# Performance work log

Hardware: AMD Instinct MI355X
Metric: run time of the kernel (lower is better)

## Reference

```python
import jax, jax.numpy as jnp
import numpy as np

V = 128
L = 128
N = 4096

_ALPHA = "abcdefghijklmnopqrstuvwxyz"
TOKENS = (list("+-*/^()=") + [f"temp_{a}" for a in _ALPHA]
          + [str(d) for d in range(10)] + [f"w{i}" for i in range(84)])
assert len(TOKENS) == V
IDX = {t: i for i, t in enumerate(TOKENS)}
TEMPS = [f"temp_{a}" for a in _ALPHA]


def _build_mask_table() -> np.ndarray:
    """mask_table[p, v] = 0 if token v is illegal after prev-token p, else 1.
    Mirrors RuleFilter.single_filter's rho for every possible prev token."""
    M = np.ones((V, V), dtype=np.float32)

    def ban(prev_tokens, banned_tokens):
        cols = [IDX[t] for t in banned_tokens]
        for p in prev_tokens:
            M[IDX[p], cols] = 0.0

    ban(list("+-*/"), list("+-*/)="))          # prev is binary op
    ban(TEMPS, list("(="))                      # prev is temp_* variable
    ban(["="], list("+-*/=)") + TEMPS)         # prev is '='
    ban(["("], list("()+-*/="))                # prev is '('
    ban([")"], list("()") + TEMPS)             # prev is ')'
    ban(["^"], list("+-*/=)"))                 # prev is '^'
    return M


def setup_inputs() -> dict:
    key = jax.random.key(0)
    logits = jax.random.normal(key, (L, N, V), dtype=jnp.float32)
    mask_table = jnp.asarray(_build_mask_table())  # (V, V) rule lookup
    return {"logits": logits, "mask_table": mask_table}


def reference(logits, mask_table):
    """logits: (L, N, V); mask_table: (V, V). Sequential rule masking:
    logits[i] *= mask_table[argmax(filtered logits[i-1])]."""
    first = logits[0]  # row 0 is never filtered

    def step(carry, cur):
        # carry: previously *filtered* logits row (N, V)
        prev_idx = jnp.argmax(carry, axis=-1)          # (N,)
        new = cur * mask_table[prev_idx]               # gather + multiply
        return new, new

    _, rest = jax.lax.scan(step, first, logits[1:])
    return jnp.concatenate([first[None], rest], axis=0)
```

## Files before the change

kernel.cpp:

```cpp
#include <hip/hip_runtime.h>


constexpr int V = 128;
constexpr int L = 128;
constexpr int N = 4096;
constexpr int D = 20;
constexpr unsigned ROWB = (unsigned)N * V * 4;

typedef __attribute__((ext_vector_type(2))) float f32x2;

__device__ __forceinline__ float wave_max_dpp(float x) {
    int v = __float_as_int(x);
    const int ninf = __float_as_int(-__builtin_inff());
#define RF_STEP(ctrl)                                                          \
    {                                                                          \
        int s = __builtin_amdgcn_update_dpp(ninf, v, ctrl, 0xf, 0xf, false);   \
        v = __float_as_int(fmaxf(__int_as_float(v), __int_as_float(s)));       \
    }
    RF_STEP(0x111)
    RF_STEP(0x112)
    RF_STEP(0x114)
    RF_STEP(0x118)
    RF_STEP(0x142)
    RF_STEP(0x143)
#undef RF_STEP
    return __int_as_float(__builtin_amdgcn_readlane(v, 63));
}

__device__ __forceinline__ int wave_argmax(f32x2 f) {
    const float bv = wave_max_dpp(fmaxf(f.x, f.y));
    unsigned long long b0 = __ballot(f.x == bv);
    unsigned long long b1 = __ballot(f.y == bv);
    int i0 = __ffsll(b0);
    int i1 = __ffsll(b1);
    int c0 = i0 ? (i0 - 1) * 2 : (1 << 30);
    int c1 = i1 ? (i1 - 1) * 2 + 1 : (1 << 30);
    return min(c0, c1);
}

__device__ __forceinline__ unsigned sel8(const unsigned* t, int j) {
    unsigned a0 = (j & 1) ? t[1] : t[0];
    unsigned a1 = (j & 1) ? t[3] : t[2];
    unsigned a2 = (j & 1) ? t[5] : t[4];
    unsigned a3 = (j & 1) ? t[7] : t[6];
    unsigned b0 = (j & 2) ? a1 : a0;
    unsigned b1 = (j & 2) ? a3 : a2;
    return (j & 4) ? b1 : b0;
}

__device__ __forceinline__ unsigned long long uniform_u64(const void* p) {
    unsigned long long x = (unsigned long long)p;
    unsigned lo = __builtin_amdgcn_readfirstlane((unsigned)x);
    unsigned hi = __builtin_amdgcn_readfirstlane((unsigned)(x >> 32));
    return ((unsigned long long)hi << 32) | lo;
}

template <int I>
struct Step {
    static __device__ __forceinline__ void run(f32x2* ring, f32x2* fbuf,
                                               const unsigned* tbl, int& prev,
                                               unsigned long long lbase,
                                               unsigned long long obase,
                                               unsigned laneoff) {
        constexpr int NW = (I <= D - 1) ? (D - 1 + I)
                         : ((I <= L - D - 1) ? (2 * D - 2) : (D - 1 + (L - 1 - I)));
        constexpr int s  = I % D;

        asm volatile("s_waitcnt vmcnt(%c2)"
                     : "+v"(ring[s])
                     : "v"(fbuf[s]), "i"(NW));

        f32x2 c = ring[s];
        f32x2 f;
        if (I == 0) {
            f = c;
        } else {
            const unsigned word  = sel8(tbl, prev >> 4);
            const unsigned fbits = (word >> ((prev & 15) * 2)) & 3u;
            f.x = (fbits & 1u) ? c.x : 0.0f;
            f.y = (fbits & 2u) ? c.y : 0.0f;
        }
        fbuf[s] = f;

        {
            unsigned voff = (unsigned)I * ROWB + laneoff;
            asm volatile("global_store_dwordx2 %0, %1, %2"
                         :
                         : "v"(voff), "v"(fbuf[s]), "s"(obase));
        }

        prev = wave_argmax(f);

        if constexpr (I + D < L) {
            unsigned voff = (unsigned)(I + D) * ROWB + laneoff;
            asm volatile("global_load_dwordx2 %0, %1, %2"
                         : "=&v"(ring[s])
                         : "v"(voff), "s"(lbase));
        }

        Step<I + 1>::run(ring, fbuf, tbl, prev, lbase, obase, laneoff);
    }
};
template <>
struct Step<L> {
    static __device__ __forceinline__ void run(f32x2*, f32x2*, const unsigned*,
                                               int&, unsigned long long,
                                               unsigned long long, unsigned) {}
};

__global__ __launch_bounds__(256, 4) void rule_filter_kernel(
    const float* __restrict__ logits,
    const float* __restrict__ mask_table,
    float* __restrict__ out)
{
    const int wave = threadIdx.x >> 6;
    const int lane = threadIdx.x & 63;
    const int n    = (blockIdx.x << 2) + wave;

    const unsigned long long lbase = uniform_u64(logits + (size_t)n * V);
    const unsigned long long obase = uniform_u64(out    + (size_t)n * V);
    const unsigned laneoff = (unsigned)lane * 8;

    unsigned tbl[8];
#pragma unroll 1
    for (int j = 0; j < 8; ++j) {
        unsigned acc = 0;
#pragma unroll
        for (int r = 0; r < 16; ++r) {
            const int p = j * 16 + r;
            float2 mv = *(const float2*)(mask_table + (size_t)p * V + lane * 2);
            acc |= ((mv.x != 0.0f ? 1u : 0u) | (mv.y != 0.0f ? 2u : 0u)) << (2 * r);
        }
        tbl[j] = acc;
    }
    asm volatile("s_waitcnt vmcnt(0)" ::: "memory");

    f32x2 ring[D];
    f32x2 fbuf[D];
#pragma unroll
    for (int r = 0; r < D; ++r) { fbuf[r].x = 0.0f; fbuf[r].y = 0.0f; }

#pragma unroll
    for (int r = 0; r < D; ++r) {
        unsigned voff = (unsigned)r * ROWB + laneoff;
        asm volatile("global_load_dwordx2 %0, %1, %2"
                     : "=&v"(ring[r])
                     : "v"(voff), "s"(lbase));
    }

    int prev = 0;
    Step<0>::run(ring, fbuf, tbl, prev, lbase, obase, laneoff);
}

extern "C" void kernel_launch(void* const* d_in, const int* in_sizes, int n_in,
                              void* d_out, int out_size, void* d_ws, size_t ws_size,
                              hipStream_t stream) {
    const float* logits     = (const float*)d_in[0];
    const float* mask_table = (const float*)d_in[1];
    float* out              = (float*)d_out;

    dim3 grid(N / 4);
    dim3 block(256);
    rule_filter_kernel<<<grid, block, 0, stream>>>(logits, mask_table, out);
}
```

Before: 439.1 us.

## Split sequential rule filter into class-argmax, chain, and apply kernels

Deduplicates mask_table rows into at most seven classes. For every logits row it computes the argmax under each class mask in a fully parallel pass, so the sequential dependency collapses to a small byte-table walk per sequence. A final streaming kernel applies the selected mask to each row. This removes the per-step latency-bound argmax chain, at the cost of reading the logits twice and needing a workspace. It also silently caps the class count at seven, so a mask table with more distinct rows would give wrong results.

New measurement: 556.8 us. 26.8% more time.

```diff
diff --git a/kernel.cpp b/kernel.cpp
--- a/kernel.cpp
+++ b/kernel.cpp
@@ -4,12 +4,22 @@
 constexpr int V = 128;
 constexpr int L = 128;
 constexpr int N = 4096;
-constexpr int D = 20;
-constexpr unsigned ROWB = (unsigned)N * V * 4;
-
-typedef __attribute__((ext_vector_type(2))) float f32x2;
-
-__device__ __forceinline__ float wave_max_dpp(float x) {
+constexpr int NROWS = L * N;
+
+struct Meta {
+    unsigned rows[8][4];
+    unsigned char slot[128];
+    unsigned nc;
+};
+constexpr size_t T1_BYTES = (size_t)NROWS * 8;
+constexpr size_t SEL_OFF  = T1_BYTES;
+constexpr size_t META_OFF = T1_BYTES + (size_t)NROWS;
+constexpr size_t WS_NEEDED = META_OFF + sizeof(Meta);
+
+typedef unsigned long long u64;
+
+
+__device__ __forceinline__ int halfmax_dpp(float x) {
     int v = __float_as_int(x);
     const int ninf = __float_as_int(-__builtin_inff());
 #define RF_STEP(ctrl)                                                          \
@@ -17,27 +27,247 @@
         int s = __builtin_amdgcn_update_dpp(ninf, v, ctrl, 0xf, 0xf, false);   \
         v = __float_as_int(fmaxf(__int_as_float(v), __int_as_float(s)));       \
     }
-    RF_STEP(0x111)
-    RF_STEP(0x112)
-    RF_STEP(0x114)
-    RF_STEP(0x118)
-    RF_STEP(0x142)
-    RF_STEP(0x143)
+    RF_STEP(0x111) RF_STEP(0x112) RF_STEP(0x114) RF_STEP(0x118) RF_STEP(0x142)
+#undef RF_STEP
+    return v;
+}
+
+__device__ __forceinline__ int argmax_half(unsigned m0, unsigned m1,
+                                           unsigned m2, unsigned m3) {
+    const int BIG = 1 << 30;
+    int c0 = m0 ? (__builtin_ctz(m0) * 4 + 0) : BIG;
+    int c1 = m1 ? (__builtin_ctz(m1) * 4 + 1) : BIG;
+    int c2 = m2 ? (__builtin_ctz(m2) * 4 + 2) : BIG;
+    int c3 = m3 ? (__builtin_ctz(m3) * 4 + 3) : BIG;
+    return min(min(c0, c1), min(c2, c3));
+}
+
+__device__ __forceinline__ unsigned sel4u(unsigned a, unsigned b, unsigned c,
+                                          unsigned d, int j) {
+    unsigned x = (j & 1) ? b : a;
+    unsigned y = (j & 1) ? d : c;
+    return (j & 2) ? y : x;
+}
+
+__device__ __forceinline__ float maskf(float x, unsigned bit) {
+    return __int_as_float(__float_as_int(x) & (0x80000000u | (0u - bit)));
+}
+
+__global__ void k0_classes(const float* __restrict__ mt, Meta* __restrict__ meta) {
+    __shared__ unsigned sb[128][4];
+    __shared__ unsigned char canon[128];
+    const int p = threadIdx.x;
+    unsigned w[4];
+#pragma unroll
+    for (int wi = 0; wi < 4; ++wi) {
+        unsigned acc = 0;
+        for (int b = 0; b < 32; ++b)
+            acc |= (mt[(size_t)p * V + wi * 32 + b] != 0.0f ? 1u : 0u) << b;
+        w[wi] = acc;
+        sb[p][wi] = acc;
+    }
+    __syncthreads();
+    int cq = p;
+    for (int q = 0; q < p; ++q) {
+        if (sb[q][0] == w[0] && sb[q][1] == w[1] && sb[q][2] == w[2] &&
+            sb[q][3] == w[3]) { cq = q; break; }
+    }
+    canon[p] = (cq == p) ? 1 : 0;
+    __syncthreads();
+    int rank = 0;
+    for (int q = 0; q < cq; ++q) rank += canon[q];
+    if (rank > 6) rank = 6;
+    meta->slot[p] = (unsigned char)rank;
+    if (cq == p && rank < 7)
+        for (int wi = 0; wi < 4; ++wi) meta->rows[rank][wi] = w[wi];
+    if (p == 0) {
+        int nc = 0;
+        for (int q = 0; q < 128; ++q) nc += canon[q];
+        meta->nc = nc > 7 ? 7 : nc;
+        for (int wi = 0; wi < 4; ++wi) meta->rows[7][wi] = 0xFFFFFFFFu;
+    }
+}
+
+__global__ __launch_bounds__(256) void k1_classargmax(
+    const float* __restrict__ logits, const Meta* __restrict__ meta,
+    u64* __restrict__ T1) {
+    const int lane = threadIdx.x & 63;
+    const int ll   = lane & 31;
+    const int half = lane >> 5;
+    const int gw   = blockIdx.x * 4 + (threadIdx.x >> 6);
+    const int NWV  = 2048 * 4;
+
+    const int nc = (int)meta->nc;
+    unsigned nib[8];
+    unsigned rw0[8], rw1[8], rw2[8], rw3[8];
+#pragma unroll
+    for (int c = 0; c < 8; ++c) {
+        rw0[c] = meta->rows[c][0]; rw1[c] = meta->rows[c][1];
+        rw2[c] = meta->rows[c][2]; rw3[c] = meta->rows[c][3];
+        unsigned word = sel4u(rw0[c], rw1[c], rw2[c], rw3[c], ll >> 3);
+        nib[c] = (word >> ((ll & 7) * 4)) & 0xFu;
+    }
+
+    const uint4* lp = (const uint4*)logits;
+
+    auto process = [&](int pw, uint4 xb) {
+        float x0 = __int_as_float(xb.x), x1 = __int_as_float(xb.y);
+        float x2 = __int_as_float(xb.z), x3 = __int_as_float(xb.w);
+        float mloc = fmaxf(fmaxf(x0, x1), fmaxf(x2, x3));
+        int mv = halfmax_dpp(mloc);
+        float bvA = __int_as_float(__builtin_amdgcn_readlane(mv, 31));
+        float bvB = __int_as_float(__builtin_amdgcn_readlane(mv, 63));
+        float bv = half ? bvB : bvA;
+        u64 e0 = __ballot(x0 == bv), e1 = __ballot(x1 == bv);
+        u64 e2 = __ballot(x2 == bv), e3 = __ballot(x3 == bv);
+        int iA7 = argmax_half((unsigned)e0, (unsigned)e1, (unsigned)e2, (unsigned)e3);
+        int iB7 = argmax_half((unsigned)(e0 >> 32), (unsigned)(e1 >> 32),
+                              (unsigned)(e2 >> 32), (unsigned)(e3 >> 32));
+        u64 accA = (u64)(unsigned)iA7 << 56;
+        u64 accB = (u64)(unsigned)iB7 << 56;
+#pragma unroll
+        for (int c = 0; c < 7; ++c) {
+            if (c < nc) {
+                bool okA = (bvA > 0.0f) &&
+                    ((sel4u(rw0[c], rw1[c], rw2[c], rw3[c], iA7 >> 5) >> (iA7 & 31)) & 1u);
+                bool okB = (bvB > 0.0f) &&
+                    ((sel4u(rw0[c], rw1[c], rw2[c], rw3[c], iB7 >> 5) >> (iB7 & 31)) & 1u);
+                int iA, iB;
+                if (okA && okB) {
+                    iA = iA7; iB = iB7;
+                } else {
+                    const unsigned nb = nib[c];
+                    float f0 = maskf(x0, nb & 1u),        f1 = maskf(x1, (nb >> 1) & 1u);
+                    float f2 = maskf(x2, (nb >> 2) & 1u), f3 = maskf(x3, (nb >> 3) & 1u);
+                    float mm = fmaxf(fmaxf(f0, f1), fmaxf(f2, f3));
+                    int mv2 = halfmax_dpp(mm);
+                    float cA = __int_as_float(__builtin_amdgcn_readlane(mv2, 31));
+                    float cB = __int_as_float(__builtin_amdgcn_readlane(mv2, 63));
+                    float cb = half ? cB : cA;
+                    u64 g0 = __ballot(f0 == cb), g1 = __ballot(f1 == cb);
+                    u64 g2 = __ballot(f2 == cb), g3 = __ballot(f3 == cb);
+                    iA = argmax_half((unsigned)g0, (unsigned)g1, (unsigned)g2, (unsigned)g3);
+                    iB = argmax_half((unsigned)(g0 >> 32), (unsigned)(g1 >> 32),
+                                     (unsigned)(g2 >> 32), (unsigned)(g3 >> 32));
+                    if (okA) iA = iA7;
+                    if (okB) iB = iB7;
+                }
+                accA |= (u64)(unsigned)iA << (8 * c);
+                accB |= (u64)(unsigned)iB << (8 * c);
+            }
+        }
+        if (lane < 2) T1[(size_t)2 * pw + lane] = lane ? accB : accA;
+    };
+
+    uint4 a = lp[((size_t)gw + 0 * NWV) * 64 + lane];
+    uint4 b = lp[((size_t)gw + 1 * NWV) * 64 + lane];
+#pragma unroll 1
+    for (int k = 0; k < 32; k += 2) {
+        uint4 n1 = a, n2 = b;
+        if (k + 2 < 32) {
+            n1 = lp[((size_t)gw + (size_t)(k + 2) * NWV) * 64 + lane];
+            n2 = lp[((size_t)gw + (size_t)(k + 3) * NWV) * 64 + lane];
+        }
+        process(gw + k * NWV, a);
+        process(gw + (k + 1) * NWV, b);
+        a = n1; b = n2;
+    }
+}
+
+__global__ __launch_bounds__(256) void k2_chain(
+    const u64* __restrict__ T1, const Meta* __restrict__ meta,
+    unsigned char* __restrict__ rowsel) {
+    __shared__ unsigned char slotl[128];
+    if (threadIdx.x < 128) slotl[threadIdx.x] = meta->slot[threadIdx.x];
+    __syncthreads();
+    const int n = blockIdx.x * 256 + threadIdx.x;
+
+    u64 cur[16], nxt[16];
+#pragma unroll
+    for (int j = 0; j < 16; ++j) cur[j] = T1[(size_t)j * N + n];
+
+    int prev = 0;
+#pragma unroll 1
+    for (int b = 0; b < 8; ++b) {
+        const int ib = b * 16;
+#pragma unroll
+        for (int j = 0; j < 16; ++j)
+            nxt[j] = (b < 7) ? T1[(size_t)(ib + 16 + j) * N + n] : 0ull;
+#pragma unroll
+        for (int j = 0; j < 16; ++j) {
+            const int i = ib + j;
+            if (i == 0) {
+                prev = (int)((cur[0] >> 56) & 0x7F);
+                rowsel[n] = (unsigned char)7;
+            } else {
+                int s = slotl[prev];
+                rowsel[(size_t)i * N + n] = (unsigned char)s;
+                prev = (int)((cur[j] >> (8 * s)) & 0x7F);
+            }
+        }
+#pragma unroll
+        for (int j = 0; j < 16; ++j) cur[j] = nxt[j];
+    }
+}
+
+__global__ __launch_bounds__(256) void k3_apply(
+    const float* __restrict__ logits, const Meta* __restrict__ meta,
+    const unsigned char* __restrict__ rowsel, float* __restrict__ out) {
+    __shared__ uint4 rowsl[8];
+    if (threadIdx.x < 8) {
+        const unsigned* r = &meta->rows[threadIdx.x][0];
+        rowsl[threadIdx.x] = make_uint4(r[0], r[1], r[2], r[3]);
+    }
+    __syncthreads();
+    const uint4* in = (const uint4*)logits;
+    uint4* o = (uint4*)out;
+    const size_t TOT = (size_t)L * N * V / 4;
+    const size_t id0 = (size_t)blockIdx.x * 256 + threadIdx.x;
+    const size_t stride = (size_t)2048 * 256;
+#pragma unroll 4
+    for (int k = 0; k < 32; ++k) {
+        size_t idx = (TOT - 1) - (id0 + (size_t)k * stride);
+        uint4 x = in[idx];
+        const int row = (int)(idx >> 5);
+        const int ll  = (int)(idx & 31);
+        const int s   = rowsel[row];
+        uint4 w = rowsl[s];
+        unsigned word = sel4u(w.x, w.y, w.z, w.w, ll >> 3);
+        unsigned nb = word >> ((ll & 7) * 4);
+        x.x &= 0x80000000u | (0u - (nb & 1u));
+        x.y &= 0x80000000u | (0u - ((nb >> 1) & 1u));
+        x.z &= 0x80000000u | (0u - ((nb >> 2) & 1u));
+        x.w &= 0x80000000u | (0u - ((nb >> 3) & 1u));
+        o[idx] = x;
+    }
+}
+
+constexpr int FD = 20;
+constexpr unsigned ROWB = (unsigned)N * V * 4;
+typedef __attribute__((ext_vector_type(2))) float f32x2;
+
+__device__ __forceinline__ float wave_max_dpp64(float x) {
+    int v = __float_as_int(x);
+    const int ninf = __float_as_int(-__builtin_inff());
+#define RF_STEP(ctrl)                                                          \
+    {                                                                          \
+        int s = __builtin_amdgcn_update_dpp(ninf, v, ctrl, 0xf, 0xf, false);   \
+        v = __float_as_int(fmaxf(__int_as_float(v), __int_as_float(s)));       \
+    }
+    RF_STEP(0x111) RF_STEP(0x112) RF_STEP(0x114) RF_STEP(0x118)
+    RF_STEP(0x142) RF_STEP(0x143)
 #undef RF_STEP
     return __int_as_float(__builtin_amdgcn_readlane(v, 63));
 }
-
-__device__ __forceinline__ int wave_argmax(f32x2 f) {
-    const float bv = wave_max_dpp(fmaxf(f.x, f.y));
-    unsigned long long b0 = __ballot(f.x == bv);
-    unsigned long long b1 = __ballot(f.y == bv);
-    int i0 = __ffsll(b0);
-    int i1 = __ffsll(b1);
+__device__ __forceinline__ int wave_argmax64(f32x2 f) {
+    const float bv = wave_max_dpp64(fmaxf(f.x, f.y));
+    u64 b0 = __ballot(f.x == bv);
+    u64 b1 = __ballot(f.y == bv);
+    int i0 = __ffsll(b0), i1 = __ffsll(b1);
     int c0 = i0 ? (i0 - 1) * 2 : (1 << 30);
     int c1 = i1 ? (i1 - 1) * 2 + 1 : (1 << 30);
     return min(c0, c1);
 }
-
 __device__ __forceinline__ unsigned sel8(const unsigned* t, int j) {
     unsigned a0 = (j & 1) ? t[1] : t[0];
     unsigned a1 = (j & 1) ? t[3] : t[2];
@@ -47,29 +277,23 @@
     unsigned b1 = (j & 2) ? a3 : a2;
     return (j & 4) ? b1 : b0;
 }
-
-__device__ __forceinline__ unsigned long long uniform_u64(const void* p) {
-    unsigned long long x = (unsigned long long)p;
+__device__ __forceinline__ u64 uniform_u64p(const void* p) {
+    u64 x = (u64)p;
     unsigned lo = __builtin_amdgcn_readfirstlane((unsigned)x);
     unsigned hi = __builtin_amdgcn_readfirstlane((unsigned)(x >> 32));
-    return ((unsigned long long)hi << 32) | lo;
-}
-
+    return ((u64)hi << 32) | lo;
+}
 template <int I>
-struct Step {
+struct FStep {
     static __device__ __forceinline__ void run(f32x2* ring, f32x2* fbuf,
                                                const unsigned* tbl, int& prev,
-                                               unsigned long long lbase,
-                                               unsigned long long obase,
+                                               u64 lbase, u64 obase,
                                                unsigned laneoff) {
-        constexpr int NW = (I <= D - 1) ? (D - 1 + I)
-                         : ((I <= L - D - 1) ? (2 * D - 2) : (D - 1 + (L - 1 - I)));
-        constexpr int s  = I % D;
-
+        constexpr int NW = (I <= FD - 1) ? (FD - 1 + I)
+                         : ((I <= L - FD - 1) ? (2 * FD - 2) : (FD - 1 + (L - 1 - I)));
+        constexpr int s = I % FD;
         asm volatile("s_waitcnt vmcnt(%c2)"
-                     : "+v"(ring[s])
-                     : "v"(fbuf[s]), "i"(NW));
-
+                     : "+v"(ring[s]) : "v"(fbuf[s]), "i"(NW));
         f32x2 c = ring[s];
         f32x2 f;
         if (I == 0) {
@@ -81,46 +305,34 @@
             f.y = (fbits & 2u) ? c.y : 0.0f;
         }
         fbuf[s] = f;
-
         {
             unsigned voff = (unsigned)I * ROWB + laneoff;
             asm volatile("global_store_dwordx2 %0, %1, %2"
-                         :
-                         : "v"(voff), "v"(fbuf[s]), "s"(obase));
-        }
-
-        prev = wave_argmax(f);
-
-        if constexpr (I + D < L) {
-            unsigned voff = (unsigned)(I + D) * ROWB + laneoff;
+                         :: "v"(voff), "v"(fbuf[s]), "s"(obase));
+        }
+        prev = wave_argmax64(f);
+        if constexpr (I + FD < L) {
+            unsigned voff = (unsigned)(I + FD) * ROWB + laneoff;
             asm volatile("global_load_dwordx2 %0, %1, %2"
-                         : "=&v"(ring[s])
-                         : "v"(voff), "s"(lbase));
-        }
-
-        Step<I + 1>::run(ring, fbuf, tbl, prev, lbase, obase, laneoff);
+                         : "=&v"(ring[s]) : "v"(voff), "s"(lbase));
+        }
+        FStep<I + 1>::run(ring, fbuf, tbl, prev, lbase, obase, laneoff);
     }
 };
 template <>
-struct Step<L> {
+struct FStep<L> {
     static __device__ __forceinline__ void run(f32x2*, f32x2*, const unsigned*,
-                                               int&, unsigned long long,
-                                               unsigned long long, unsigned) {}
+                                               int&, u64, u64, unsigned) {}
 };
-
-__global__ __launch_bounds__(256, 4) void rule_filter_kernel(
-    const float* __restrict__ logits,
-    const float* __restrict__ mask_table,
-    float* __restrict__ out)
-{
+__global__ __launch_bounds__(256, 4) void rule_filter_fused(
+    const float* __restrict__ logits, const float* __restrict__ mask_table,
+    float* __restrict__ out) {
     const int wave = threadIdx.x >> 6;
     const int lane = threadIdx.x & 63;
     const int n    = (blockIdx.x << 2) + wave;
-
-    const unsigned long long lbase = uniform_u64(logits + (size_t)n * V);
-    const unsigned long long obase = uniform_u64(out    + (size_t)n * V);
+    const u64 lbase = uniform_u64p(logits + (size_t)n * V);
+    const u64 obase = uniform_u64p(out    + (size_t)n * V);
     const unsigned laneoff = (unsigned)lane * 8;
-
     unsigned tbl[8];
 #pragma unroll 1
     for (int j = 0; j < 8; ++j) {
@@ -134,22 +346,18 @@
         tbl[j] = acc;
     }
     asm volatile("s_waitcnt vmcnt(0)" ::: "memory");
-
-    f32x2 ring[D];
-    f32x2 fbuf[D];
-#pragma unroll
-    for (int r = 0; r < D; ++r) { fbuf[r].x = 0.0f; fbuf[r].y = 0.0f; }
-
-#pragma unroll
-    for (int r = 0; r < D; ++r) {
+    f32x2 ring[FD];
+    f32x2 fbuf[FD];
+#pragma unroll
+    for (int r = 0; r < FD; ++r) { fbuf[r].x = 0.0f; fbuf[r].y = 0.0f; }
+#pragma unroll
+    for (int r = 0; r < FD; ++r) {
         unsigned voff = (unsigned)r * ROWB + laneoff;
         asm volatile("global_load_dwordx2 %0, %1, %2"
-                     : "=&v"(ring[r])
-                     : "v"(voff), "s"(lbase));
-    }
-
+                     : "=&v"(ring[r]) : "v"(voff), "s"(lbase));
+    }
     int prev = 0;
-    Step<0>::run(ring, fbuf, tbl, prev, lbase, obase, laneoff);
+    FStep<0>::run(ring, fbuf, tbl, prev, lbase, obase, laneoff);
 }
 
 extern "C" void kernel_launch(void* const* d_in, const int* in_sizes, int n_in,
@@ -159,7 +367,18 @@
     const float* mask_table = (const float*)d_in[1];
     float* out              = (float*)d_out;
 
-    dim3 grid(N / 4);
-    dim3 block(256);
-    rule_filter_kernel<<<grid, block, 0, stream>>>(logits, mask_table, out);
-}
+    if (d_ws != nullptr && ws_size >= WS_NEEDED) {
+        unsigned char* ws = (unsigned char*)d_ws;
+        u64* T1            = (u64*)ws;
+        unsigned char* sel = ws + SEL_OFF;
+        Meta* meta         = (Meta*)(ws + META_OFF);
+        k0_classes<<<1, 128, 0, stream>>>(mask_table, meta);
+        k1_classargmax<<<2048, 256, 0, stream>>>(logits, meta, T1);
+        k2_chain<<<16, 256, 0, stream>>>(T1, meta, sel);
+        k3_apply<<<2048, 256, 0, stream>>>(logits, meta, sel, out);
+    } else {
+        dim3 grid(N / 4);
+        dim3 block(256);
+        rule_filter_fused<<<grid, block, 0, stream>>>(logits, mask_table, out);
+    }
+}
```

## Split each sequence into producer argmax wave and consumer store wave via LDS flags

Applied to the files above, without the earlier changes.

Each column n now gets a block of two waves instead of one wave. The producer wave computes the masked row and its argmax and publishes prev indices through LDS flags. The consumer wave, which independently loads the same logits, spins on those flags, applies the mask and stores the output. The aim is to take store traffic and register pressure off the argmax-dependent critical chain, using a 16-slot ring with 15-deep prefetch. In exchange, every logit row is loaded twice (L2 may serve the repeat), the consumer busy-waits on LDS, and the grid grows to 4096 small blocks.

Result: slower. 479.5 us (+9.2%).

```diff
diff --git a/kernel.cpp b/kernel.cpp
--- a/kernel.cpp
+++ b/kernel.cpp
@@ -4,10 +4,12 @@
 constexpr int V = 128;
 constexpr int L = 128;
 constexpr int N = 4096;
-constexpr int D = 20;
+constexpr int D  = 15;
+constexpr int RD = 16;
 constexpr unsigned ROWB = (unsigned)N * V * 4;
 
 typedef __attribute__((ext_vector_type(2))) float f32x2;
+typedef unsigned long long u64;
 
 __device__ __forceinline__ float wave_max_dpp(float x) {
     int v = __float_as_int(x);
@@ -17,22 +19,17 @@
         int s = __builtin_amdgcn_update_dpp(ninf, v, ctrl, 0xf, 0xf, false);   \
         v = __float_as_int(fmaxf(__int_as_float(v), __int_as_float(s)));       \
     }
-    RF_STEP(0x111)
-    RF_STEP(0x112)
-    RF_STEP(0x114)
-    RF_STEP(0x118)
-    RF_STEP(0x142)
-    RF_STEP(0x143)
+    RF_STEP(0x111) RF_STEP(0x112) RF_STEP(0x114) RF_STEP(0x118)
+    RF_STEP(0x142) RF_STEP(0x143)
 #undef RF_STEP
     return __int_as_float(__builtin_amdgcn_readlane(v, 63));
 }
 
 __device__ __forceinline__ int wave_argmax(f32x2 f) {
     const float bv = wave_max_dpp(fmaxf(f.x, f.y));
-    unsigned long long b0 = __ballot(f.x == bv);
-    unsigned long long b1 = __ballot(f.y == bv);
-    int i0 = __ffsll(b0);
-    int i1 = __ffsll(b1);
+    u64 b0 = __ballot(f.x == bv);
+    u64 b1 = __ballot(f.y == bv);
+    int i0 = __ffsll(b0), i1 = __ffsll(b1);
     int c0 = i0 ? (i0 - 1) * 2 : (1 << 30);
     int c1 = i1 ? (i1 - 1) * 2 + 1 : (1 << 30);
     return min(c0, c1);
@@ -48,77 +45,114 @@
     return (j & 4) ? b1 : b0;
 }
 
-__device__ __forceinline__ unsigned long long uniform_u64(const void* p) {
-    unsigned long long x = (unsigned long long)p;
+__device__ __forceinline__ u64 uniform_u64(const void* p) {
+    u64 x = (u64)p;
     unsigned lo = __builtin_amdgcn_readfirstlane((unsigned)x);
     unsigned hi = __builtin_amdgcn_readfirstlane((unsigned)(x >> 32));
-    return ((unsigned long long)hi << 32) | lo;
-}
-
-template <int I>
-struct Step {
-    static __device__ __forceinline__ void run(f32x2* ring, f32x2* fbuf,
-                                               const unsigned* tbl, int& prev,
-                                               unsigned long long lbase,
-                                               unsigned long long obase,
-                                               unsigned laneoff) {
-        constexpr int NW = (I <= D - 1) ? (D - 1 + I)
-                         : ((I <= L - D - 1) ? (2 * D - 2) : (D - 1 + (L - 1 - I)));
-        constexpr int s  = I % D;
-
-        asm volatile("s_waitcnt vmcnt(%c2)"
-                     : "+v"(ring[s])
-                     : "v"(fbuf[s]), "i"(NW));
-
-        f32x2 c = ring[s];
-        f32x2 f;
-        if (I == 0) {
-            f = c;
-        } else {
-            const unsigned word  = sel8(tbl, prev >> 4);
-            const unsigned fbits = (word >> ((prev & 15) * 2)) & 3u;
-            f.x = (fbits & 1u) ? c.x : 0.0f;
-            f.y = (fbits & 2u) ? c.y : 0.0f;
-        }
-        fbuf[s] = f;
-
-        {
-            unsigned voff = (unsigned)I * ROWB + laneoff;
-            asm volatile("global_store_dwordx2 %0, %1, %2"
-                         :
-                         : "v"(voff), "v"(fbuf[s]), "s"(obase));
-        }
-
-        prev = wave_argmax(f);
-
-        if constexpr (I + D < L) {
-            unsigned voff = (unsigned)(I + D) * ROWB + laneoff;
+    return ((u64)hi << 32) | lo;
+}
+
+template <bool PROD, int PH, int J>
+struct Walk {
+    static constexpr int  NW    = PROD ? ((PH == 2 && J > 0) ? (15 - J) : 15)
+                                       : ((PH == 0) ? (15 + J)
+                                          : ((PH == 2 && J > 0) ? (30 - J) : 30));
+    static constexpr bool PF    = (PH != 2) || (J == 0);
+    static constexpr bool FIRST = (PH == 0 && J == 0);
+    static constexpr bool LAST  = (PH == 2 && J == 15);
+    static constexpr int  rs    = J & 15;
+    static constexpr int  ps    = (J + D) & 15;
+
+    static __device__ __forceinline__ void run(f32x2* ring, const unsigned* tbl,
+                                               int& prev, int irow, unsigned ibase,
+                                               u64 lbase, u64 obase,
+                                               volatile unsigned* flg, int lane) {
+        if constexpr (PF) {
+            unsigned voff = ibase + (unsigned)(J + D) * ROWB;
             asm volatile("global_load_dwordx2 %0, %1, %2"
-                         : "=&v"(ring[s])
+                         : "=&v"(ring[ps])
                          : "v"(voff), "s"(lbase));
         }
 
-        Step<I + 1>::run(ring, fbuf, tbl, prev, lbase, obase, laneoff);
+        asm volatile("s_waitcnt vmcnt(%c1)" : "+v"(ring[rs]) : "i"(NW));
+
+        f32x2 c = ring[rs];
+
+        if constexpr (PROD) {
+            f32x2 f;
+            if constexpr (FIRST) {
+                f = c;
+            } else {
+                unsigned word = sel8(tbl, prev >> 4);
+                unsigned fb   = (word >> ((prev & 15) * 2)) & 3u;
+                f.x = (fb & 1u) ? c.x : 0.0f;
+                f.y = (fb & 2u) ? c.y : 0.0f;
+            }
+            if constexpr (!LAST) {
+                prev = wave_argmax(f);
+                if (lane == 0) flg[irow + J + 1] = 0x100u | (unsigned)prev;
+            }
+        } else {
+            f32x2 f;
+            if constexpr (FIRST) {
+                f = c;
+            } else {
+                unsigned v;
+                while ((v = flg[irow + J]) == 0u) {}
+                int pv = (int)(v & 127u);
+                unsigned word = sel8(tbl, pv >> 4);
+                unsigned fb   = (word >> ((pv & 15) * 2)) & 3u;
+                f.x = (fb & 1u) ? c.x : 0.0f;
+                f.y = (fb & 2u) ? c.y : 0.0f;
+            }
+            ring[rs] = f;
+            unsigned voff = ibase + (unsigned)J * ROWB;
+            asm volatile("global_store_dwordx2 %0, %1, %2"
+                         :: "v"(voff), "v"(ring[rs]), "s"(obase));
+        }
+
+        Walk<PROD, PH, J + 1>::run(ring, tbl, prev, irow, ibase, lbase, obase,
+                                   flg, lane);
     }
 };
-template <>
-struct Step<L> {
-    static __device__ __forceinline__ void run(f32x2*, f32x2*, const unsigned*,
-                                               int&, unsigned long long,
-                                               unsigned long long, unsigned) {}
+template <bool PROD, int PH>
+struct Walk<PROD, PH, 16> {
+    static __device__ __forceinline__ void run(f32x2*, const unsigned*, int&,
+                                               int, unsigned, u64, u64,
+                                               volatile unsigned*, int) {}
 };
 
-__global__ __launch_bounds__(256, 4) void rule_filter_kernel(
+template <bool PROD>
+__device__ __forceinline__ void walk_all(f32x2* ring, const unsigned* tbl,
+                                         u64 lbase, u64 obase,
+                                         volatile unsigned* flg,
+                                         int lane, unsigned laneoff) {
+    int prev = 0;
+    int irow = 0;
+    unsigned ibase = laneoff;
+    Walk<PROD, 0, 0>::run(ring, tbl, prev, irow, ibase, lbase, obase, flg, lane);
+    irow = 16; ibase += 16u * ROWB;
+#pragma unroll 1
+    for (int m = 0; m < 6; ++m) {
+        Walk<PROD, 1, 0>::run(ring, tbl, prev, irow, ibase, lbase, obase, flg, lane);
+        irow += 16; ibase += 16u * ROWB;
+    }
+    Walk<PROD, 2, 0>::run(ring, tbl, prev, irow, ibase, lbase, obase, flg, lane);
+}
+
+__global__ __launch_bounds__(128, 8) void rule_filter_kernel(
     const float* __restrict__ logits,
     const float* __restrict__ mask_table,
     float* __restrict__ out)
 {
-    const int wave = threadIdx.x >> 6;
+    __shared__ unsigned flgs[132];
+
+    const int h    = threadIdx.x >> 6;
     const int lane = threadIdx.x & 63;
-    const int n    = (blockIdx.x << 2) + wave;
-
-    const unsigned long long lbase = uniform_u64(logits + (size_t)n * V);
-    const unsigned long long obase = uniform_u64(out    + (size_t)n * V);
+    const int n    = blockIdx.x;
+
+    const u64 lbase = uniform_u64(logits + (size_t)n * V);
+    const u64 obase = uniform_u64(out    + (size_t)n * V);
     const unsigned laneoff = (unsigned)lane * 8;
 
     unsigned tbl[8];
@@ -133,13 +167,13 @@
         }
         tbl[j] = acc;
     }
+
+    flgs[threadIdx.x] = 0;
+    if (threadIdx.x < 4) flgs[128 + threadIdx.x] = 0;
+    __syncthreads();
     asm volatile("s_waitcnt vmcnt(0)" ::: "memory");
 
-    f32x2 ring[D];
-    f32x2 fbuf[D];
-#pragma unroll
-    for (int r = 0; r < D; ++r) { fbuf[r].x = 0.0f; fbuf[r].y = 0.0f; }
-
+    f32x2 ring[RD];
 #pragma unroll
     for (int r = 0; r < D; ++r) {
         unsigned voff = (unsigned)r * ROWB + laneoff;
@@ -148,8 +182,11 @@
                      : "v"(voff), "s"(lbase));
     }
 
-    int prev = 0;
-    Step<0>::run(ring, fbuf, tbl, prev, lbase, obase, laneoff);
+    volatile unsigned* flg = flgs;
+    if (h == 0) walk_all<true >(ring, tbl, lbase, obase, flg, lane, laneoff);
+    else        walk_all<false>(ring, tbl, lbase, obase, flg, lane, laneoff);
+
+    asm volatile("s_waitcnt vmcnt(0)" ::: "memory");
 }
 
 extern "C" void kernel_launch(void* const* d_in, const int* in_sizes, int n_in,
@@ -159,7 +196,7 @@
     const float* mask_table = (const float*)d_in[1];
     float* out              = (float*)d_out;
 
-    dim3 grid(N / 4);
-    dim3 block(256);
+    dim3 grid(N);
+    dim3 block(128);
     rule_filter_kernel<<<grid, block, 0, stream>>>(logits, mask_table, out);
 }
```
